# Kernel tuning notes

Measured on AMD Instinct MI355X. Metric: run time of the kernel, lower is better.

## Reference

```python
import jax, jax.numpy as jnp
import numpy as np

N_NODES = 20000
DEG = 6
E = N_NODES * DEG  # 120000 edges == line-graph nodes
D_NODE, D_EDGE = 64, 16
HID, OUT = 128, 128
EPS = 1e-5


def setup_inputs() -> dict:
    key = jax.random.key(0)
    ks = jax.random.split(key, 8)
    rng = np.random.default_rng(0)
    # graph: each node is the source of DEG edges (direction='out' -> index_r = edge_index[0])
    src = np.repeat(np.arange(N_NODES), DEG)
    dst = rng.integers(0, N_NODES, E)
    edge_index = np.stack([src, dst]).astype(np.int64)
    # two_step_index: ordered pairs of distinct edges sharing a source node
    # (bipartite 2-hop, self loops removed), then GATConv add_self_loops re-appends (i,i)
    ii, jj = np.meshgrid(np.arange(DEG), np.arange(DEG), indexing='ij')
    off = ~np.eye(DEG, dtype=bool)
    ii, jj = ii[off], jj[off]  # DEG*(DEG-1) within-group pairs
    base = (np.arange(N_NODES) * DEG)[:, None]
    s2 = np.concatenate([(base + ii[None, :]).ravel(), np.arange(E)])
    d2 = np.concatenate([(base + jj[None, :]).ravel(), np.arange(E)])
    index_2step = np.stack([s2, d2]).astype(np.int64)  # [2, 720000]
    d_in = D_NODE + D_EDGE
    return {
        "edge_attr": jax.random.normal(ks[0], (E, D_EDGE), jnp.float32),
        "node_attr": jax.random.normal(ks[1], (N_NODES, D_NODE), jnp.float32),
        "bn0_g": jnp.ones((d_in,), jnp.float32),
        "bn0_b": jnp.zeros((d_in,), jnp.float32),
        "W1": jax.random.normal(ks[2], (d_in, HID), jnp.float32) / np.sqrt(d_in).astype(np.float32),
        "bn1_g": jnp.ones((HID,), jnp.float32),
        "bn1_b": jnp.zeros((HID,), jnp.float32),
        "Wg": jax.random.normal(ks[3], (HID, OUT), jnp.float32) / np.sqrt(HID).astype(np.float32),
        "att_src": jax.random.normal(ks[4], (OUT,), jnp.float32) * 0.1,
        "att_dst": jax.random.normal(ks[5], (OUT,), jnp.float32) * 0.1,
        "gat_bias": jnp.zeros((OUT,), jnp.float32),
        "bnf_g": jnp.ones((OUT,), jnp.float32),
        "bnf_b": jnp.zeros((OUT,), jnp.float32),
        "edge_index": jnp.asarray(edge_index),
        "index_2step": jnp.asarray(index_2step),
        "num_nodes": N_NODES,
    }


def batch_norm(x, g, b):
    # training-mode BatchNorm1d (biased variance), like the torch module default
    mu = x.mean(0)
    var = x.var(0)
    return (x - mu) * jax.lax.rsqrt(var + EPS) * g + b


def reference(edge_attr, node_attr, bn0_g, bn0_b, W1, bn1_g, bn1_b,
              Wg, att_src, att_dst, gat_bias, bnf_g, bnf_b,
              edge_index, index_2step, num_nodes):
    index_r = edge_index[0]  # [E] source node of each edge (direction='out')
    # h0: per-edge concat of source-node attrs and edge attrs  [E, Dn+De]
    h0 = jnp.concatenate([node_attr[index_r], edge_attr], axis=1)
    # linear encoder: BN -> Linear(no bias) -> BN -> ReLU (dropout p=0)
    h1 = jax.nn.relu(batch_norm(batch_norm(h0, bn0_g, bn0_b) @ W1, bn1_g, bn1_b))
    # --- GATConv (heads=1) on the line graph given by index_2step ---
    E_ = h1.shape[0]
    x = h1 @ Wg                 # [E, OUT]
    a_src = x @ att_src         # [E]
    a_dst = x @ att_dst         # [E]
    s, d = index_2step[0], index_2step[1]
    e = jax.nn.leaky_relu(a_src[s] + a_dst[d], 0.2)          # [E2]
    e = e - jax.ops.segment_max(e, d, num_segments=E_)[d]    # stable edge-softmax
    ex = jnp.exp(e)
    alpha = ex / (jax.ops.segment_sum(ex, d, num_segments=E_)[d] + 1e-16)
    h2 = jax.ops.segment_sum(alpha[:, None] * x[s], d, num_segments=E_) + gat_bias
    # --- global_add_pool keyed by source node id, then final BatchNorm ---
    h3 = jax.ops.segment_sum(h2, index_r, num_segments=num_nodes)  # [N, OUT]
    return batch_norm(h3, bnf_g, bnf_b)
```

## Files before the change

kernel.cpp:

```cpp
#include <hip/hip_runtime.h>

#define N_NODES 20000
#define DEG 6
#define E_EDGES 120000
#define EPS_BN 1e-5f

#define WS_S0SUM 0
#define WS_S0SQ  80
#define WS_S1SUM 160
#define WS_S1SQ  1184
#define WS_FSUM  2208
#define WS_FSQ   3232
#define WS_STATS_FLOATS 4256
#define WS_WT1   4256
#define WS_WGT   10400

#define LDA0 104
#define LDH1 136

typedef float f32x4 __attribute__((ext_vector_type(4)));
typedef short bf16x8 __attribute__((ext_vector_type(8)));

__device__ __forceinline__ unsigned short f2bf(float f) {
  unsigned u = __float_as_uint(f);
  u += 0x7fffu + ((u >> 16) & 1u);
  return (unsigned short)(u >> 16);
}
__device__ __forceinline__ unsigned pack2bf(float a, float b) {
  return (unsigned)f2bf(a) | ((unsigned)f2bf(b) << 16);
}

__global__ __launch_bounds__(256) void k0_prep(
    const float* __restrict__ W1, const float* __restrict__ Wg,
    float* __restrict__ ws) {
  short* wt1 = (short*)(ws + WS_WT1);
  short* wgt = (short*)(ws + WS_WGT);
  const int t0 = blockIdx.x * 256 + threadIdx.x;
  for (int i = t0; i < 128 * 96; i += 32 * 256) {
    int col = i / 96, k = i % 96;
    wt1[i] = (k < 80) ? (short)f2bf(W1[k * 128 + col]) : (short)0;
  }
  for (int i = t0; i < 128 * 128; i += 32 * 256) {
    int col = i >> 7, k = i & 127;
    wgt[i] = (short)f2bf(Wg[k * 128 + col]);
  }
}

__global__ __launch_bounds__(256) void k1_bn0_stats(
    const float* __restrict__ node_attr, const float* __restrict__ edge_attr,
    float* __restrict__ ws) {
  __shared__ float red[256];
  const int t = threadIdx.x;
  const int b = blockIdx.x;
  if (b < 128) {
    const int c = t & 63, rl = t >> 6;
    float s = 0.f, q = 0.f;
    for (int row = b * 4 + rl; row < N_NODES; row += 512) {
      float v = node_attr[row * 64 + c];
      s += v; q += v * v;
    }
    red[t] = s;
    __syncthreads();
    if (t < 64) atomicAdd(&ws[WS_S0SUM + t], red[t] + red[t + 64] + red[t + 128] + red[t + 192]);
    __syncthreads();
    red[t] = q;
    __syncthreads();
    if (t < 64) atomicAdd(&ws[WS_S0SQ + t], red[t] + red[t + 64] + red[t + 128] + red[t + 192]);
  } else {
    const int c = t & 15, rl = t >> 4;
    float s = 0.f, q = 0.f;
    for (int row = (b - 128) * 16 + rl; row < E_EDGES; row += 2048) {
      float v = edge_attr[row * 16 + c];
      s += v; q += v * v;
    }
    red[t] = s;
    __syncthreads();
    if (t < 16) {
      float tot = 0.f;
      #pragma unroll
      for (int k = 0; k < 16; ++k) tot += red[t + 16 * k];
      atomicAdd(&ws[WS_S0SUM + 64 + t], tot);
    }
    __syncthreads();
    red[t] = q;
    __syncthreads();
    if (t < 16) {
      float tot = 0.f;
      #pragma unroll
      for (int k = 0; k < 16; ++k) tot += red[t + 16 * k];
      atomicAdd(&ws[WS_S0SQ + 64 + t], tot);
    }
  }
}

__global__ __launch_bounds__(256, 2) void k2_bn1_stats(
    const float* __restrict__ node_attr, const float* __restrict__ edge_attr,
    const float* __restrict__ bn0_g, const float* __restrict__ bn0_b,
    float* __restrict__ ws) {
  __shared__ short h0s[48 * LDA0];
  __shared__ float sc0[80], sh0[80];
  const int t = threadIdx.x;
  if (t < 80) {
    float cnt = (t < 64) ? (float)N_NODES : (float)E_EDGES;
    float mu = ws[WS_S0SUM + t] / cnt;
    float var = ws[WS_S0SQ + t] / cnt - mu * mu;
    float sc = bn0_g[t] * rsqrtf(var + EPS_BN);
    sc0[t] = sc; sh0[t] = bn0_b[t] - mu * sc;
  }
  const int l = t & 63, wid = t >> 6;
  const int lm = l & 15, lq = l >> 4;
  const int Nb = wid * 32;
  const short* wt1 = (const short*)(ws + WS_WT1);
  bf16x8 w1f[2][3];
  #pragma unroll
  for (int nt = 0; nt < 2; ++nt)
    #pragma unroll
    for (int ks = 0; ks < 3; ++ks)
      w1f[nt][ks] = *(const bf16x8*)&wt1[(Nb + nt * 16 + lm) * 96 + ks * 32 + lq * 8];
  __syncthreads();
  const int ebase = blockIdx.x * 48;
  for (int i = t; i < 48 * 40; i += 256) {
    int row = i / 40, pc = i % 40, c = pc * 2;
    int ge = ebase + row;
    float a, b;
    if (c < 64) {
      const float* p = node_attr + (ge / DEG) * 64 + c;
      a = p[0]; b = p[1];
    } else {
      const float* p = edge_attr + ge * 16 + (c - 64);
      a = p[0]; b = p[1];
    }
    a = a * sc0[c] + sh0[c];
    b = b * sc0[c + 1] + sh0[c + 1];
    *(unsigned*)&h0s[row * LDA0 + c] = pack2bf(a, b);
  }
  for (int i = t; i < 48 * 8; i += 256) {
    int row = i >> 3, pc = i & 7;
    *(unsigned*)&h0s[row * LDA0 + 80 + pc * 2] = 0u;
  }
  __syncthreads();
  f32x4 acc[3][2] = {};
  #pragma unroll
  for (int ks = 0; ks < 3; ++ks) {
    bf16x8 a[3];
    #pragma unroll
    for (int mt = 0; mt < 3; ++mt)
      a[mt] = *(const bf16x8*)&h0s[(mt * 16 + lm) * LDA0 + ks * 32 + lq * 8];
    #pragma unroll
    for (int mt = 0; mt < 3; ++mt)
      #pragma unroll
      for (int nt = 0; nt < 2; ++nt)
        acc[mt][nt] = __builtin_amdgcn_mfma_f32_16x16x32_bf16(a[mt], w1f[nt][ks], acc[mt][nt], 0, 0, 0);
  }
  const int set = blockIdx.x & 7;
  #pragma unroll
  for (int nt = 0; nt < 2; ++nt) {
    float s = 0.f, q = 0.f;
    #pragma unroll
    for (int mt = 0; mt < 3; ++mt)
      #pragma unroll
      for (int r = 0; r < 4; ++r) {
        float v = acc[mt][nt][r];
        s += v; q += v * v;
      }
    s += __shfl_xor(s, 16); s += __shfl_xor(s, 32);
    q += __shfl_xor(q, 16); q += __shfl_xor(q, 32);
    if (l < 16) {
      int col = Nb + nt * 16 + lm;
      atomicAdd(&ws[WS_S1SUM + set * 128 + col], s);
      atomicAdd(&ws[WS_S1SQ + set * 128 + col], q);
    }
  }
}

__global__ __launch_bounds__(256, 2) void k3_fused(
    const float* __restrict__ node_attr, const float* __restrict__ edge_attr,
    const float* __restrict__ bn0_g, const float* __restrict__ bn0_b,
    const float* __restrict__ bn1_g, const float* __restrict__ bn1_b,
    const float* __restrict__ att_src, const float* __restrict__ att_dst,
    const float* __restrict__ gat_bias,
    float* __restrict__ out, float* __restrict__ ws) {
  __shared__ short h0s[48 * LDA0];
  __shared__ short h1s[48 * LDH1];
  __shared__ float sc0[80], sh0[80];
  __shared__ float sc1[128], sh1[128];
  __shared__ float asP[4][48], adP[4][48];
  __shared__ float asS[48], adS[48], wS[48];
  __shared__ float alphaL[48][6];
  __shared__ float h3L[8 * 128];
  __shared__ float red[8][128];

  const int t = threadIdx.x;
  if (t < 80) {
    float cnt = (t < 64) ? (float)N_NODES : (float)E_EDGES;
    float mu = ws[WS_S0SUM + t] / cnt;
    float var = ws[WS_S0SQ + t] / cnt - mu * mu;
    float sc = bn0_g[t] * rsqrtf(var + EPS_BN);
    sc0[t] = sc; sh0[t] = bn0_b[t] - mu * sc;
  }
  if (t < 128) {
    float s = 0.f, q = 0.f;
    #pragma unroll
    for (int st = 0; st < 8; ++st) {
      s += ws[WS_S1SUM + st * 128 + t];
      q += ws[WS_S1SQ + st * 128 + t];
    }
    const float invE = 1.f / (float)E_EDGES;
    float mu = s * invE;
    float var = q * invE - mu * mu;
    float sc = bn1_g[t] * rsqrtf(var + EPS_BN);
    sc1[t] = sc; sh1[t] = bn1_b[t] - mu * sc;
  }
  *(f32x4*)&h3L[t * 4] = (f32x4){0.f, 0.f, 0.f, 0.f};

  const int l = t & 63, wid = t >> 6;
  const int lm = l & 15, lq = l >> 4;
  const int Nb = wid * 32;
  const short* wt1 = (const short*)(ws + WS_WT1);
  const short* wgt = (const short*)(ws + WS_WGT);
  const int ebase = blockIdx.x * 48;
  __syncthreads();

  {
    bf16x8 w1f[2][3];
    #pragma unroll
    for (int nt = 0; nt < 2; ++nt)
      #pragma unroll
      for (int ks = 0; ks < 3; ++ks)
        w1f[nt][ks] = *(const bf16x8*)&wt1[(Nb + nt * 16 + lm) * 96 + ks * 32 + lq * 8];
    float scc[2], shc[2];
    #pragma unroll
    for (int nt = 0; nt < 2; ++nt) {
      int col = Nb + nt * 16 + lm;
      scc[nt] = sc1[col]; shc[nt] = sh1[col];
    }
    for (int i = t; i < 48 * 40; i += 256) {
      int row = i / 40, pc = i % 40, c = pc * 2;
      int ge = ebase + row;
      float a, b;
      if (c < 64) {
        const float* p = node_attr + (ge / DEG) * 64 + c;
        a = p[0]; b = p[1];
      } else {
        const float* p = edge_attr + ge * 16 + (c - 64);
        a = p[0]; b = p[1];
      }
      a = a * sc0[c] + sh0[c];
      b = b * sc0[c + 1] + sh0[c + 1];
      *(unsigned*)&h0s[row * LDA0 + c] = pack2bf(a, b);
    }
    for (int i = t; i < 48 * 8; i += 256) {
      int row = i >> 3, pc = i & 7;
      *(unsigned*)&h0s[row * LDA0 + 80 + pc * 2] = 0u;
    }
    __syncthreads();
    f32x4 acc1[3][2] = {};
    #pragma unroll
    for (int ks = 0; ks < 3; ++ks) {
      bf16x8 a[3];
      #pragma unroll
      for (int mt = 0; mt < 3; ++mt)
        a[mt] = *(const bf16x8*)&h0s[(mt * 16 + lm) * LDA0 + ks * 32 + lq * 8];
      #pragma unroll
      for (int mt = 0; mt < 3; ++mt)
        #pragma unroll
        for (int nt = 0; nt < 2; ++nt)
          acc1[mt][nt] = __builtin_amdgcn_mfma_f32_16x16x32_bf16(a[mt], w1f[nt][ks], acc1[mt][nt], 0, 0, 0);
    }
    #pragma unroll
    for (int mt = 0; mt < 3; ++mt)
      #pragma unroll
      for (int nt = 0; nt < 2; ++nt)
        #pragma unroll
        for (int r = 0; r < 4; ++r) {
          int row = mt * 16 + lq * 4 + r;
          int col = Nb + nt * 16 + lm;
          float v = fmaxf(acc1[mt][nt][r] * scc[nt] + shc[nt], 0.f);
          h1s[row * LDH1 + col] = (short)f2bf(v);
        }
  }
  __syncthreads();

  bf16x8 wgf[2][4];
  #pragma unroll
  for (int nt = 0; nt < 2; ++nt)
    #pragma unroll
    for (int ks = 0; ks < 4; ++ks)
      wgf[nt][ks] = *(const bf16x8*)&wgt[(Nb + nt * 16 + lm) * 128 + ks * 32 + lq * 8];
  float atS[2], atD[2];
  #pragma unroll
  for (int nt = 0; nt < 2; ++nt) {
    int col = Nb + nt * 16 + lm;
    atS[nt] = att_src[col]; atD[nt] = att_dst[col];
  }
  f32x4 acc2[3][2] = {};
  #pragma unroll
  for (int ks = 0; ks < 4; ++ks) {
    bf16x8 a[3];
    #pragma unroll
    for (int mt = 0; mt < 3; ++mt)
      a[mt] = *(const bf16x8*)&h1s[(mt * 16 + lm) * LDH1 + ks * 32 + lq * 8];
    #pragma unroll
    for (int mt = 0; mt < 3; ++mt)
      #pragma unroll
      for (int nt = 0; nt < 2; ++nt)
        acc2[mt][nt] = __builtin_amdgcn_mfma_f32_16x16x32_bf16(a[mt], wgf[nt][ks], acc2[mt][nt], 0, 0, 0);
  }
  {
    float ps[3][4], pd[3][4];
    #pragma unroll
    for (int mt = 0; mt < 3; ++mt)
      #pragma unroll
      for (int r = 0; r < 4; ++r) {
        ps[mt][r] = acc2[mt][0][r] * atS[0] + acc2[mt][1][r] * atS[1];
        pd[mt][r] = acc2[mt][0][r] * atD[0] + acc2[mt][1][r] * atD[1];
      }
    #pragma unroll
    for (int off = 1; off < 16; off <<= 1)
      #pragma unroll
      for (int mt = 0; mt < 3; ++mt)
        #pragma unroll
        for (int r = 0; r < 4; ++r) {
          ps[mt][r] += __shfl_xor(ps[mt][r], off);
          pd[mt][r] += __shfl_xor(pd[mt][r], off);
        }
    if (lm == 0) {
      #pragma unroll
      for (int mt = 0; mt < 3; ++mt)
        #pragma unroll
        for (int r = 0; r < 4; ++r) {
          int row = mt * 16 + lq * 4 + r;
          asP[wid][row] = ps[mt][r];
          adP[wid][row] = pd[mt][r];
        }
    }
  }
  __syncthreads();
  if (t < 48) {
    asS[t] = asP[0][t] + asP[1][t] + asP[2][t] + asP[3][t];
    adS[t] = adP[0][t] + adP[1][t] + adP[2][t] + adP[3][t];
  }
  __syncthreads();
  if (t < 48) {
    int n = t / 6, nb6 = n * 6;
    float ad = adS[t];
    float s6[6], m = -1e30f;
    #pragma unroll
    for (int i = 0; i < 6; ++i) {
      float s = asS[nb6 + i] + ad;
      s = (s > 0.f) ? s : 0.2f * s;
      s6[i] = s; m = fmaxf(m, s);
    }
    float ssum = 0.f, ex[6];
    #pragma unroll
    for (int i = 0; i < 6; ++i) { ex[i] = __expf(s6[i] - m); ssum += ex[i]; }
    float inv = 1.f / (ssum + 1e-16f);
    #pragma unroll
    for (int i = 0; i < 6; ++i) alphaL[t][i] = ex[i] * inv;
  }
  __syncthreads();
  if (t < 48) {
    int n = t / 6, i = t % 6;
    float w = 0.f;
    #pragma unroll
    for (int j = 0; j < 6; ++j) w += alphaL[n * 6 + j][i];
    wS[t] = w;
  }
  __syncthreads();
  #pragma unroll
  for (int mt = 0; mt < 3; ++mt)
    #pragma unroll
    for (int r = 0; r < 4; ++r) {
      int row = mt * 16 + lq * 4 + r;
      float w = wS[row];
      int nl = row / 6;
      #pragma unroll
      for (int nt = 0; nt < 2; ++nt)
        atomicAdd(&h3L[nl * 128 + Nb + nt * 16 + lm], w * acc2[mt][nt][r]);
    }
  __syncthreads();
  const int c4 = (t & 31) * 4, nslot = t >> 5;
  f32x4 v = *(f32x4*)&h3L[nslot * 128 + c4];
  const f32x4 gb = *(const f32x4*)&gat_bias[c4];
  v[0] += 6.f * gb[0]; v[1] += 6.f * gb[1];
  v[2] += 6.f * gb[2]; v[3] += 6.f * gb[3];
  *(f32x4*)&out[(blockIdx.x * 8 + nslot) * 128 + c4] = v;
  const int set = blockIdx.x & 7;
  #pragma unroll
  for (int j = 0; j < 4; ++j) red[nslot][c4 + j] = v[j];
  __syncthreads();
  if (t < 128) {
    float s = 0.f;
    #pragma unroll
    for (int k = 0; k < 8; ++k) s += red[k][t];
    atomicAdd(&ws[WS_FSUM + set * 128 + t], s);
  }
  __syncthreads();
  #pragma unroll
  for (int j = 0; j < 4; ++j) red[nslot][c4 + j] = v[j] * v[j];
  __syncthreads();
  if (t < 128) {
    float s = 0.f;
    #pragma unroll
    for (int k = 0; k < 8; ++k) s += red[k][t];
    atomicAdd(&ws[WS_FSQ + set * 128 + t], s);
  }
}

__global__ __launch_bounds__(256) void k4_final(
    float* __restrict__ out, const float* __restrict__ ws,
    const float* __restrict__ bnf_g, const float* __restrict__ bnf_b) {
  int idx4 = blockIdx.x * 256 + threadIdx.x;
  if (idx4 >= N_NODES * 128 / 4) return;
  int c0 = (idx4 & 31) << 2;
  float4 v = ((float4*)out)[idx4];
  float4 fsv = {0.f, 0.f, 0.f, 0.f}, fqv = {0.f, 0.f, 0.f, 0.f};
  #pragma unroll
  for (int s = 0; s < 8; ++s) {
    float4 a = *(const float4*)&ws[WS_FSUM + s * 128 + c0];
    float4 b = *(const float4*)&ws[WS_FSQ + s * 128 + c0];
    fsv.x += a.x; fsv.y += a.y; fsv.z += a.z; fsv.w += a.w;
    fqv.x += b.x; fqv.y += b.y; fqv.z += b.z; fqv.w += b.w;
  }
  float4 g4 = *(const float4*)&bnf_g[c0];
  float4 b4 = *(const float4*)&bnf_b[c0];
  const float invN = 1.f / (float)N_NODES;
  float mu, var, sc;
  mu = fsv.x * invN; var = fqv.x * invN - mu * mu; sc = g4.x * rsqrtf(var + EPS_BN);
  v.x = (v.x - mu) * sc + b4.x;
  mu = fsv.y * invN; var = fqv.y * invN - mu * mu; sc = g4.y * rsqrtf(var + EPS_BN);
  v.y = (v.y - mu) * sc + b4.y;
  mu = fsv.z * invN; var = fqv.z * invN - mu * mu; sc = g4.z * rsqrtf(var + EPS_BN);
  v.z = (v.z - mu) * sc + b4.z;
  mu = fsv.w * invN; var = fqv.w * invN - mu * mu; sc = g4.w * rsqrtf(var + EPS_BN);
  v.w = (v.w - mu) * sc + b4.w;
  ((float4*)out)[idx4] = v;
}

extern "C" void kernel_launch(void* const* d_in, const int* in_sizes, int n_in,
                              void* d_out, int out_size, void* d_ws, size_t ws_size,
                              hipStream_t stream) {
  const float* edge_attr = (const float*)d_in[0];
  const float* node_attr = (const float*)d_in[1];
  const float* bn0_g = (const float*)d_in[2];
  const float* bn0_b = (const float*)d_in[3];
  const float* W1    = (const float*)d_in[4];
  const float* bn1_g = (const float*)d_in[5];
  const float* bn1_b = (const float*)d_in[6];
  const float* Wg    = (const float*)d_in[7];
  const float* att_src = (const float*)d_in[8];
  const float* att_dst = (const float*)d_in[9];
  const float* gat_bias = (const float*)d_in[10];
  const float* bnf_g = (const float*)d_in[11];
  const float* bnf_b = (const float*)d_in[12];
  float* ws = (float*)d_ws;
  float* out = (float*)d_out;

  hipMemsetAsync(d_ws, 0, WS_STATS_FLOATS * sizeof(float), stream);
  k0_prep<<<32, 256, 0, stream>>>(W1, Wg, ws);
  k1_bn0_stats<<<256, 256, 0, stream>>>(node_attr, edge_attr, ws);
  k2_bn1_stats<<<E_EDGES / 48, 256, 0, stream>>>(node_attr, edge_attr, bn0_g, bn0_b, ws);
  k3_fused<<<E_EDGES / 48, 256, 0, stream>>>(node_attr, edge_attr, bn0_g, bn0_b,
                                             bn1_g, bn1_b, att_src, att_dst, gat_bias,
                                             out, ws);
  k4_final<<<2500, 256, 0, stream>>>(out, ws, bnf_g, bnf_b);
}
```

Measured before the change: 250.0 us.

## Fold BN0 into W1, double tile size, split final stats into separate pass

BN0 scale is folded into the bf16 W1 weights and its shift into a precomputed bias, so the staging loops no longer apply per-element normalization. Each node's attributes are staged once and shared by its six edges through a row/6 index, and the block tile grows from 48 to 96 edges. BN1 finalization moves into a tiny kernel, and the final BN statistics come from a separate reduction pass over the output instead of atomics in the fused kernel. The cost is two extra launches and an extra read of the output, plus more LDS per block, which may lower occupancy.

```diff
diff --git a/kernel.cpp b/kernel.cpp
--- a/kernel.cpp
+++ b/kernel.cpp
@@ -4,19 +4,22 @@
 #define DEG 6
 #define E_EDGES 120000
 #define EPS_BN 1e-5f
+#define NBLK 1250
+#define EB 96
+#define NB 16
 
 #define WS_S0SUM 0
 #define WS_S0SQ  80
-#define WS_S1SUM 160
-#define WS_S1SQ  1184
-#define WS_FSUM  2208
-#define WS_FSQ   3232
-#define WS_STATS_FLOATS 4256
-#define WS_WT1   4256
-#define WS_WGT   10400
-
-#define LDA0 104
-#define LDH1 136
+#define WS_BIAS1 160
+#define WS_S1SUM 288
+#define WS_S1SQ  1312
+#define WS_SC1M  2336
+#define WS_SH1M  2464
+#define WS_FSUM  2592
+#define WS_FSQ   2720
+#define WS_STATS_FLOATS 2848
+#define WS_WT1   2848
+#define WS_WGT   8992
 
 typedef float f32x4 __attribute__((ext_vector_type(4)));
 typedef short bf16x8 __attribute__((ext_vector_type(8)));
@@ -28,22 +31,6 @@
 }
 __device__ __forceinline__ unsigned pack2bf(float a, float b) {
   return (unsigned)f2bf(a) | ((unsigned)f2bf(b) << 16);
-}
-
-__global__ __launch_bounds__(256) void k0_prep(
-    const float* __restrict__ W1, const float* __restrict__ Wg,
-    float* __restrict__ ws) {
-  short* wt1 = (short*)(ws + WS_WT1);
-  short* wgt = (short*)(ws + WS_WGT);
-  const int t0 = blockIdx.x * 256 + threadIdx.x;
-  for (int i = t0; i < 128 * 96; i += 32 * 256) {
-    int col = i / 96, k = i % 96;
-    wt1[i] = (k < 80) ? (short)f2bf(W1[k * 128 + col]) : (short)0;
-  }
-  for (int i = t0; i < 128 * 128; i += 32 * 256) {
-    int col = i >> 7, k = i & 127;
-    wgt[i] = (short)f2bf(Wg[k * 128 + col]);
-  }
 }
 
 __global__ __launch_bounds__(256) void k1_bn0_stats(
@@ -93,74 +80,103 @@
   }
 }
 
+__global__ __launch_bounds__(256) void k0_fold(
+    const float* __restrict__ W1, const float* __restrict__ Wg,
+    const float* __restrict__ bn0_g, const float* __restrict__ bn0_b,
+    float* __restrict__ ws) {
+  short* wt1 = (short*)(ws + WS_WT1);
+  short* wgt = (short*)(ws + WS_WGT);
+  const int t0 = blockIdx.x * 256 + threadIdx.x;
+  for (int i = t0; i < 128 * 96; i += 32 * 256) {
+    int n = i / 96, k = i % 96;
+    float v = 0.f;
+    if (k < 80) {
+      float cnt = (k < 64) ? (float)N_NODES : (float)E_EDGES;
+      float mu = ws[WS_S0SUM + k] / cnt;
+      float var = ws[WS_S0SQ + k] / cnt - mu * mu;
+      v = W1[k * 128 + n] * (bn0_g[k] * rsqrtf(var + EPS_BN));
+    }
+    wt1[i] = (short)f2bf(v);
+  }
+  for (int i = t0; i < 128 * 128; i += 32 * 256) {
+    int n = i >> 7, k = i & 127;
+    wgt[i] = (short)f2bf(Wg[k * 128 + n]);
+  }
+  if (blockIdx.x == 0 && threadIdx.x < 128) {
+    int n = threadIdx.x;
+    float s = 0.f;
+    for (int k = 0; k < 80; ++k) {
+      float cnt = (k < 64) ? (float)N_NODES : (float)E_EDGES;
+      float mu = ws[WS_S0SUM + k] / cnt;
+      float var = ws[WS_S0SQ + k] / cnt - mu * mu;
+      float sc = bn0_g[k] * rsqrtf(var + EPS_BN);
+      s += (bn0_b[k] - mu * sc) * W1[k * 128 + n];
+    }
+    ws[WS_BIAS1 + n] = s;
+  }
+}
+
+#define STAGE_INPUTS()                                                         \
+  {                                                                            \
+    int i = t;                                                                 \
+    int row = i >> 4, c4 = (i & 15) << 2;                                      \
+    float4 v = *(const float4*)&node_attr[(size_t)(g * NB + row) * 64 + c4];   \
+    *(uint2*)&n0s[row * 72 + c4] = make_uint2(pack2bf(v.x, v.y), pack2bf(v.z, v.w)); \
+  }                                                                            \
+  for (int i = t; i < EB * 4; i += 256) {                                      \
+    int row = i >> 2, c4 = (i & 3) << 2;                                       \
+    float4 v = *(const float4*)&edge_attr[(size_t)(g * EB + row) * 16 + c4];   \
+    *(uint2*)&e0s[row * 24 + c4] = make_uint2(pack2bf(v.x, v.y), pack2bf(v.z, v.w)); \
+  }                                                                            \
+  if (t < 8) zpad[t] = 0;
+
+#define GEMM1_CORE(acc1)                                                       \
+  _Pragma("unroll")                                                            \
+  for (int ks = 0; ks < 3; ++ks) {                                             \
+    bf16x8 bb0 = *(const bf16x8*)&wt1[(Nb + lm) * 96 + ks * 32 + lq * 8];      \
+    bf16x8 bb1 = *(const bf16x8*)&wt1[(Nb + 16 + lm) * 96 + ks * 32 + lq * 8]; \
+    _Pragma("unroll")                                                          \
+    for (int mt = 0; mt < 6; ++mt) {                                           \
+      const short* ap;                                                         \
+      if (ks < 2) ap = &n0s[rowdiv6[mt] * 72 + ks * 32 + lq * 8];              \
+      else ap = (lq < 2) ? &e0s[(mt * 16 + lm) * 24 + lq * 8] : zpad;          \
+      bf16x8 a = *(const bf16x8*)ap;                                           \
+      acc1[mt][0] = __builtin_amdgcn_mfma_f32_16x16x32_bf16(a, bb0, acc1[mt][0], 0, 0, 0); \
+      acc1[mt][1] = __builtin_amdgcn_mfma_f32_16x16x32_bf16(a, bb1, acc1[mt][1], 0, 0, 0); \
+    }                                                                          \
+  }
+
 __global__ __launch_bounds__(256, 2) void k2_bn1_stats(
     const float* __restrict__ node_attr, const float* __restrict__ edge_attr,
-    const float* __restrict__ bn0_g, const float* __restrict__ bn0_b,
     float* __restrict__ ws) {
-  __shared__ short h0s[48 * LDA0];
-  __shared__ float sc0[80], sh0[80];
+  __shared__ __align__(16) short n0s[16 * 72];
+  __shared__ __align__(16) short e0s[96 * 24];
+  __shared__ __align__(16) short zpad[8];
   const int t = threadIdx.x;
-  if (t < 80) {
-    float cnt = (t < 64) ? (float)N_NODES : (float)E_EDGES;
-    float mu = ws[WS_S0SUM + t] / cnt;
-    float var = ws[WS_S0SQ + t] / cnt - mu * mu;
-    float sc = bn0_g[t] * rsqrtf(var + EPS_BN);
-    sc0[t] = sc; sh0[t] = bn0_b[t] - mu * sc;
-  }
+  const int g = blockIdx.x;
   const int l = t & 63, wid = t >> 6;
   const int lm = l & 15, lq = l >> 4;
   const int Nb = wid * 32;
   const short* wt1 = (const short*)(ws + WS_WT1);
-  bf16x8 w1f[2][3];
-  #pragma unroll
-  for (int nt = 0; nt < 2; ++nt)
-    #pragma unroll
-    for (int ks = 0; ks < 3; ++ks)
-      w1f[nt][ks] = *(const bf16x8*)&wt1[(Nb + nt * 16 + lm) * 96 + ks * 32 + lq * 8];
-  __syncthreads();
-  const int ebase = blockIdx.x * 48;
-  for (int i = t; i < 48 * 40; i += 256) {
-    int row = i / 40, pc = i % 40, c = pc * 2;
-    int ge = ebase + row;
-    float a, b;
-    if (c < 64) {
-      const float* p = node_attr + (ge / DEG) * 64 + c;
-      a = p[0]; b = p[1];
-    } else {
-      const float* p = edge_attr + ge * 16 + (c - 64);
-      a = p[0]; b = p[1];
-    }
-    a = a * sc0[c] + sh0[c];
-    b = b * sc0[c + 1] + sh0[c + 1];
-    *(unsigned*)&h0s[row * LDA0 + c] = pack2bf(a, b);
-  }
-  for (int i = t; i < 48 * 8; i += 256) {
-    int row = i >> 3, pc = i & 7;
-    *(unsigned*)&h0s[row * LDA0 + 80 + pc * 2] = 0u;
-  }
-  __syncthreads();
-  f32x4 acc[3][2] = {};
-  #pragma unroll
-  for (int ks = 0; ks < 3; ++ks) {
-    bf16x8 a[3];
-    #pragma unroll
-    for (int mt = 0; mt < 3; ++mt)
-      a[mt] = *(const bf16x8*)&h0s[(mt * 16 + lm) * LDA0 + ks * 32 + lq * 8];
-    #pragma unroll
-    for (int mt = 0; mt < 3; ++mt)
-      #pragma unroll
-      for (int nt = 0; nt < 2; ++nt)
-        acc[mt][nt] = __builtin_amdgcn_mfma_f32_16x16x32_bf16(a[mt], w1f[nt][ks], acc[mt][nt], 0, 0, 0);
-  }
-  const int set = blockIdx.x & 7;
+  int rowdiv6[6];
+  #pragma unroll
+  for (int mt = 0; mt < 6; ++mt) rowdiv6[mt] = (mt * 16 + lm) / 6;
+  float bias1c[2];
+  bias1c[0] = ws[WS_BIAS1 + Nb + lm];
+  bias1c[1] = ws[WS_BIAS1 + Nb + 16 + lm];
+  STAGE_INPUTS();
+  __syncthreads();
+  f32x4 acc1[6][2] = {};
+  GEMM1_CORE(acc1);
+  const int set = g & 7;
   #pragma unroll
   for (int nt = 0; nt < 2; ++nt) {
     float s = 0.f, q = 0.f;
     #pragma unroll
-    for (int mt = 0; mt < 3; ++mt)
+    for (int mt = 0; mt < 6; ++mt)
       #pragma unroll
       for (int r = 0; r < 4; ++r) {
-        float v = acc[mt][nt][r];
+        float v = acc1[mt][nt][r] + bias1c[nt];
         s += v; q += v * v;
       }
     s += __shfl_xor(s, 16); s += __shfl_xor(s, 32);
@@ -173,176 +189,120 @@
   }
 }
 
+__global__ __launch_bounds__(128) void k2b_finalize(
+    const float* __restrict__ bn1_g, const float* __restrict__ bn1_b,
+    float* __restrict__ ws) {
+  const int t = threadIdx.x;
+  float s = 0.f, q = 0.f;
+  #pragma unroll
+  for (int st = 0; st < 8; ++st) {
+    s += ws[WS_S1SUM + st * 128 + t];
+    q += ws[WS_S1SQ + st * 128 + t];
+  }
+  const float invE = 1.f / (float)E_EDGES;
+  float mu = s * invE;
+  float var = q * invE - mu * mu;
+  float sc1 = bn1_g[t] * rsqrtf(var + EPS_BN);
+  float sh1 = bn1_b[t] - mu * sc1;
+  ws[WS_SC1M + t] = sc1;
+  ws[WS_SH1M + t] = ws[WS_BIAS1 + t] * sc1 + sh1;
+}
+
 __global__ __launch_bounds__(256, 2) void k3_fused(
     const float* __restrict__ node_attr, const float* __restrict__ edge_attr,
-    const float* __restrict__ bn0_g, const float* __restrict__ bn0_b,
-    const float* __restrict__ bn1_g, const float* __restrict__ bn1_b,
     const float* __restrict__ att_src, const float* __restrict__ att_dst,
     const float* __restrict__ gat_bias,
     float* __restrict__ out, float* __restrict__ ws) {
-  __shared__ short h0s[48 * LDA0];
-  __shared__ short h1s[48 * LDH1];
-  __shared__ float sc0[80], sh0[80];
-  __shared__ float sc1[128], sh1[128];
-  __shared__ float asP[4][48], adP[4][48];
-  __shared__ float asS[48], adS[48], wS[48];
-  __shared__ float alphaL[48][6];
-  __shared__ float h3L[8 * 128];
-  __shared__ float red[8][128];
+  __shared__ __align__(16) short n0s[16 * 72];
+  __shared__ __align__(16) short e0s[96 * 24];
+  __shared__ __align__(16) short zpad[8];
+  __shared__ __align__(16) short h1s[96 * 136];
+  __shared__ float asP[4][96], adP[4][96];
+  __shared__ float asS[96], adS[96], wS[96];
+  __shared__ float alphaL[96][6];
+  __shared__ float h3L[16 * 128];
 
   const int t = threadIdx.x;
-  if (t < 80) {
-    float cnt = (t < 64) ? (float)N_NODES : (float)E_EDGES;
-    float mu = ws[WS_S0SUM + t] / cnt;
-    float var = ws[WS_S0SQ + t] / cnt - mu * mu;
-    float sc = bn0_g[t] * rsqrtf(var + EPS_BN);
-    sc0[t] = sc; sh0[t] = bn0_b[t] - mu * sc;
-  }
-  if (t < 128) {
-    float s = 0.f, q = 0.f;
-    #pragma unroll
-    for (int st = 0; st < 8; ++st) {
-      s += ws[WS_S1SUM + st * 128 + t];
-      q += ws[WS_S1SQ + st * 128 + t];
-    }
-    const float invE = 1.f / (float)E_EDGES;
-    float mu = s * invE;
-    float var = q * invE - mu * mu;
-    float sc = bn1_g[t] * rsqrtf(var + EPS_BN);
-    sc1[t] = sc; sh1[t] = bn1_b[t] - mu * sc;
-  }
-  *(f32x4*)&h3L[t * 4] = (f32x4){0.f, 0.f, 0.f, 0.f};
-
+  const int g = blockIdx.x;
   const int l = t & 63, wid = t >> 6;
   const int lm = l & 15, lq = l >> 4;
   const int Nb = wid * 32;
   const short* wt1 = (const short*)(ws + WS_WT1);
   const short* wgt = (const short*)(ws + WS_WGT);
-  const int ebase = blockIdx.x * 48;
-  __syncthreads();
-
+  int rowdiv6[6];
+  #pragma unroll
+  for (int mt = 0; mt < 6; ++mt) rowdiv6[mt] = (mt * 16 + lm) / 6;
+  float sc1c[2], sh1c[2], atS[2], atD[2];
+  #pragma unroll
+  for (int nt = 0; nt < 2; ++nt) {
+    int col = Nb + nt * 16 + lm;
+    sc1c[nt] = ws[WS_SC1M + col];
+    sh1c[nt] = ws[WS_SH1M + col];
+    atS[nt] = att_src[col];
+    atD[nt] = att_dst[col];
+  }
+  #pragma unroll
+  for (int j = 0; j < 2; ++j)
+    *(f32x4*)&h3L[(t + j * 256) * 4] = (f32x4){0.f, 0.f, 0.f, 0.f};
+  STAGE_INPUTS();
+  __syncthreads();
   {
-    bf16x8 w1f[2][3];
-    #pragma unroll
-    for (int nt = 0; nt < 2; ++nt)
-      #pragma unroll
-      for (int ks = 0; ks < 3; ++ks)
-        w1f[nt][ks] = *(const bf16x8*)&wt1[(Nb + nt * 16 + lm) * 96 + ks * 32 + lq * 8];
-    float scc[2], shc[2];
-    #pragma unroll
-    for (int nt = 0; nt < 2; ++nt) {
-      int col = Nb + nt * 16 + lm;
-      scc[nt] = sc1[col]; shc[nt] = sh1[col];
-    }
-    for (int i = t; i < 48 * 40; i += 256) {
-      int row = i / 40, pc = i % 40, c = pc * 2;
-      int ge = ebase + row;
-      float a, b;
-      if (c < 64) {
-        const float* p = node_attr + (ge / DEG) * 64 + c;
-        a = p[0]; b = p[1];
-      } else {
-        const float* p = edge_attr + ge * 16 + (c - 64);
-        a = p[0]; b = p[1];
-      }
-      a = a * sc0[c] + sh0[c];
-      b = b * sc0[c + 1] + sh0[c + 1];
-      *(unsigned*)&h0s[row * LDA0 + c] = pack2bf(a, b);
-    }
-    for (int i = t; i < 48 * 8; i += 256) {
-      int row = i >> 3, pc = i & 7;
-      *(unsigned*)&h0s[row * LDA0 + 80 + pc * 2] = 0u;
-    }
-    __syncthreads();
-    f32x4 acc1[3][2] = {};
-    #pragma unroll
-    for (int ks = 0; ks < 3; ++ks) {
-      bf16x8 a[3];
-      #pragma unroll
-      for (int mt = 0; mt < 3; ++mt)
-        a[mt] = *(const bf16x8*)&h0s[(mt * 16 + lm) * LDA0 + ks * 32 + lq * 8];
-      #pragma unroll
-      for (int mt = 0; mt < 3; ++mt)
-        #pragma unroll
-        for (int nt = 0; nt < 2; ++nt)
-          acc1[mt][nt] = __builtin_amdgcn_mfma_f32_16x16x32_bf16(a[mt], w1f[nt][ks], acc1[mt][nt], 0, 0, 0);
-    }
-    #pragma unroll
-    for (int mt = 0; mt < 3; ++mt)
+    f32x4 acc1[6][2] = {};
+    GEMM1_CORE(acc1);
+    #pragma unroll
+    for (int mt = 0; mt < 6; ++mt)
       #pragma unroll
       for (int nt = 0; nt < 2; ++nt)
         #pragma unroll
         for (int r = 0; r < 4; ++r) {
           int row = mt * 16 + lq * 4 + r;
           int col = Nb + nt * 16 + lm;
-          float v = fmaxf(acc1[mt][nt][r] * scc[nt] + shc[nt], 0.f);
-          h1s[row * LDH1 + col] = (short)f2bf(v);
+          float v = fmaxf(acc1[mt][nt][r] * sc1c[nt] + sh1c[nt], 0.f);
+          h1s[row * 136 + col] = (short)f2bf(v);
         }
   }
   __syncthreads();
-
-  bf16x8 wgf[2][4];
-  #pragma unroll
-  for (int nt = 0; nt < 2; ++nt)
-    #pragma unroll
-    for (int ks = 0; ks < 4; ++ks)
-      wgf[nt][ks] = *(const bf16x8*)&wgt[(Nb + nt * 16 + lm) * 128 + ks * 32 + lq * 8];
-  float atS[2], atD[2];
-  #pragma unroll
-  for (int nt = 0; nt < 2; ++nt) {
-    int col = Nb + nt * 16 + lm;
-    atS[nt] = att_src[col]; atD[nt] = att_dst[col];
-  }
-  f32x4 acc2[3][2] = {};
+  f32x4 acc2[6][2] = {};
   #pragma unroll
   for (int ks = 0; ks < 4; ++ks) {
-    bf16x8 a[3];
-    #pragma unroll
-    for (int mt = 0; mt < 3; ++mt)
-      a[mt] = *(const bf16x8*)&h1s[(mt * 16 + lm) * LDH1 + ks * 32 + lq * 8];
-    #pragma unroll
-    for (int mt = 0; mt < 3; ++mt)
-      #pragma unroll
-      for (int nt = 0; nt < 2; ++nt)
-        acc2[mt][nt] = __builtin_amdgcn_mfma_f32_16x16x32_bf16(a[mt], wgf[nt][ks], acc2[mt][nt], 0, 0, 0);
+    bf16x8 bb0 = *(const bf16x8*)&wgt[(Nb + lm) * 128 + ks * 32 + lq * 8];
+    bf16x8 bb1 = *(const bf16x8*)&wgt[(Nb + 16 + lm) * 128 + ks * 32 + lq * 8];
+    #pragma unroll
+    for (int mt = 0; mt < 6; ++mt) {
+      bf16x8 a = *(const bf16x8*)&h1s[(mt * 16 + lm) * 136 + ks * 32 + lq * 8];
+      acc2[mt][0] = __builtin_amdgcn_mfma_f32_16x16x32_bf16(a, bb0, acc2[mt][0], 0, 0, 0);
+      acc2[mt][1] = __builtin_amdgcn_mfma_f32_16x16x32_bf16(a, bb1, acc2[mt][1], 0, 0, 0);
+    }
   }
   {
-    float ps[3][4], pd[3][4];
-    #pragma unroll
-    for (int mt = 0; mt < 3; ++mt)
+    float ps, pd;
+    #pragma unroll
+    for (int mt = 0; mt < 6; ++mt)
       #pragma unroll
       for (int r = 0; r < 4; ++r) {
-        ps[mt][r] = acc2[mt][0][r] * atS[0] + acc2[mt][1][r] * atS[1];
-        pd[mt][r] = acc2[mt][0][r] * atD[0] + acc2[mt][1][r] * atD[1];
+        ps = acc2[mt][0][r] * atS[0] + acc2[mt][1][r] * atS[1];
+        pd = acc2[mt][0][r] * atD[0] + acc2[mt][1][r] * atD[1];
+        #pragma unroll
+        for (int off = 1; off < 16; off <<= 1) {
+          ps += __shfl_xor(ps, off);
+          pd += __shfl_xor(pd, off);
+        }
+        if (lm == 0) {
+          int row = mt * 16 + lq * 4 + r;
+          asP[wid][row] = ps;
+          adP[wid][row] = pd;
+        }
       }
-    #pragma unroll
-    for (int off = 1; off < 16; off <<= 1)
-      #pragma unroll
-      for (int mt = 0; mt < 3; ++mt)
-        #pragma unroll
-        for (int r = 0; r < 4; ++r) {
-          ps[mt][r] += __shfl_xor(ps[mt][r], off);
-          pd[mt][r] += __shfl_xor(pd[mt][r], off);
-        }
-    if (lm == 0) {
-      #pragma unroll
-      for (int mt = 0; mt < 3; ++mt)
-        #pragma unroll
-        for (int r = 0; r < 4; ++r) {
-          int row = mt * 16 + lq * 4 + r;
-          asP[wid][row] = ps[mt][r];
-          adP[wid][row] = pd[mt][r];
-        }
-    }
-  }
-  __syncthreads();
-  if (t < 48) {
+  }
+  __syncthreads();
+  if (t < 96) {
     asS[t] = asP[0][t] + asP[1][t] + asP[2][t] + asP[3][t];
     adS[t] = adP[0][t] + adP[1][t] + adP[2][t] + adP[3][t];
   }
   __syncthreads();
-  if (t < 48) {
-    int n = t / 6, nb6 = n * 6;
+  if (t < 96) {
+    int n = t / 6;
+    int nb6 = n * 6;
     float ad = adS[t];
     float s6[6], m = -1e30f;
     #pragma unroll
@@ -359,7 +319,7 @@
     for (int i = 0; i < 6; ++i) alphaL[t][i] = ex[i] * inv;
   }
   __syncthreads();
-  if (t < 48) {
+  if (t < 96) {
     int n = t / 6, i = t % 6;
     float w = 0.f;
     #pragma unroll
@@ -368,7 +328,7 @@
   }
   __syncthreads();
   #pragma unroll
-  for (int mt = 0; mt < 3; ++mt)
+  for (int mt = 0; mt < 6; ++mt)
     #pragma unroll
     for (int r = 0; r < 4; ++r) {
       int row = mt * 16 + lq * 4 + r;
@@ -379,49 +339,61 @@
         atomicAdd(&h3L[nl * 128 + Nb + nt * 16 + lm], w * acc2[mt][nt][r]);
     }
   __syncthreads();
-  const int c4 = (t & 31) * 4, nslot = t >> 5;
-  f32x4 v = *(f32x4*)&h3L[nslot * 128 + c4];
-  const f32x4 gb = *(const f32x4*)&gat_bias[c4];
-  v[0] += 6.f * gb[0]; v[1] += 6.f * gb[1];
-  v[2] += 6.f * gb[2]; v[3] += 6.f * gb[3];
-  *(f32x4*)&out[(blockIdx.x * 8 + nslot) * 128 + c4] = v;
-  const int set = blockIdx.x & 7;
-  #pragma unroll
-  for (int j = 0; j < 4; ++j) red[nslot][c4 + j] = v[j];
+  #pragma unroll
+  for (int j = 0; j < 2; ++j) {
+    int idx = t + j * 256;
+    int nslot = idx >> 5, c4 = (idx & 31) << 2;
+    f32x4 v = *(f32x4*)&h3L[nslot * 128 + c4];
+    const f32x4 gb = *(const f32x4*)&gat_bias[c4];
+    v[0] += 6.f * gb[0]; v[1] += 6.f * gb[1];
+    v[2] += 6.f * gb[2]; v[3] += 6.f * gb[3];
+    *(f32x4*)&out[(size_t)(g * NB + nslot) * 128 + c4] = v;
+  }
+}
+
+__global__ __launch_bounds__(256) void k4a_stats(
+    const float* __restrict__ out, float* __restrict__ ws) {
+  __shared__ float red[8][128];
+  const int t = threadIdx.x;
+  const int c4 = (t & 31) << 2, rl = t >> 5;
+  float fs[4] = {0.f, 0.f, 0.f, 0.f}, fq[4] = {0.f, 0.f, 0.f, 0.f};
+  for (int r = blockIdx.x * 8 + rl; r < N_NODES; r += 128 * 8) {
+    float4 v = *(const float4*)&out[(size_t)r * 128 + c4];
+    fs[0] += v.x; fq[0] += v.x * v.x;
+    fs[1] += v.y; fq[1] += v.y * v.y;
+    fs[2] += v.z; fq[2] += v.z * v.z;
+    fs[3] += v.w; fq[3] += v.w * v.w;
+  }
+  #pragma unroll
+  for (int j = 0; j < 4; ++j) red[rl][c4 + j] = fs[j];
   __syncthreads();
   if (t < 128) {
     float s = 0.f;
     #pragma unroll
     for (int k = 0; k < 8; ++k) s += red[k][t];
-    atomicAdd(&ws[WS_FSUM + set * 128 + t], s);
-  }
-  __syncthreads();
-  #pragma unroll
-  for (int j = 0; j < 4; ++j) red[nslot][c4 + j] = v[j] * v[j];
+    atomicAdd(&ws[WS_FSUM + t], s);
+  }
+  __syncthreads();
+  #pragma unroll
+  for (int j = 0; j < 4; ++j) red[rl][c4 + j] = fq[j];
   __syncthreads();
   if (t < 128) {
     float s = 0.f;
     #pragma unroll
     for (int k = 0; k < 8; ++k) s += red[k][t];
-    atomicAdd(&ws[WS_FSQ + set * 128 + t], s);
-  }
-}
-
-__global__ __launch_bounds__(256) void k4_final(
+    atomicAdd(&ws[WS_FSQ + t], s);
+  }
+}
+
+__global__ __launch_bounds__(256) void k4b_apply(
     float* __restrict__ out, const float* __restrict__ ws,
     const float* __restrict__ bnf_g, const float* __restrict__ bnf_b) {
   int idx4 = blockIdx.x * 256 + threadIdx.x;
   if (idx4 >= N_NODES * 128 / 4) return;
   int c0 = (idx4 & 31) << 2;
   float4 v = ((float4*)out)[idx4];
-  float4 fsv = {0.f, 0.f, 0.f, 0.f}, fqv = {0.f, 0.f, 0.f, 0.f};
-  #pragma unroll
-  for (int s = 0; s < 8; ++s) {
-    float4 a = *(const float4*)&ws[WS_FSUM + s * 128 + c0];
-    float4 b = *(const float4*)&ws[WS_FSQ + s * 128 + c0];
-    fsv.x += a.x; fsv.y += a.y; fsv.z += a.z; fsv.w += a.w;
-    fqv.x += b.x; fqv.y += b.y; fqv.z += b.z; fqv.w += b.w;
-  }
+  float4 fsv = *(const float4*)&ws[WS_FSUM + c0];
+  float4 fqv = *(const float4*)&ws[WS_FSQ + c0];
   float4 g4 = *(const float4*)&bnf_g[c0];
   float4 b4 = *(const float4*)&bnf_b[c0];
   const float invN = 1.f / (float)N_NODES;
@@ -457,11 +429,12 @@
   float* out = (float*)d_out;
 
   hipMemsetAsync(d_ws, 0, WS_STATS_FLOATS * sizeof(float), stream);
-  k0_prep<<<32, 256, 0, stream>>>(W1, Wg, ws);
   k1_bn0_stats<<<256, 256, 0, stream>>>(node_attr, edge_attr, ws);
-  k2_bn1_stats<<<E_EDGES / 48, 256, 0, stream>>>(node_attr, edge_attr, bn0_g, bn0_b, ws);
-  k3_fused<<<E_EDGES / 48, 256, 0, stream>>>(node_attr, edge_attr, bn0_g, bn0_b,
-                                             bn1_g, bn1_b, att_src, att_dst, gat_bias,
-                                             out, ws);
-  k4_final<<<2500, 256, 0, stream>>>(out, ws, bnf_g, bnf_b);
-}
+  k0_fold<<<32, 256, 0, stream>>>(W1, Wg, bn0_g, bn0_b, ws);
+  k2_bn1_stats<<<NBLK, 256, 0, stream>>>(node_attr, edge_attr, ws);
+  k2b_finalize<<<1, 128, 0, stream>>>(bn1_g, bn1_b, ws);
+  k3_fused<<<NBLK, 256, 0, stream>>>(node_attr, edge_attr, att_src, att_dst,
+                                     gat_bias, out, ws);
+  k4a_stats<<<128, 256, 0, stream>>>(out, ws);
+  k4b_apply<<<2500, 256, 0, stream>>>(out, ws, bnf_g, bnf_b);
+}
```

Result: no change. 249.8 us (-0.1%).
